# Kernel tuning notes

Hardware: AMD Instinct MI355X
Metric: run time of the kernel (lower is better)

Reference implementation:

```python
import jax, jax.numpy as jnp
import numpy as np

E = 8          # num_ensemble
S = 512        # state_dim
A = 64         # action_dim
H = 2048       # hidden_dim
L = 3          # num_layers - 1 residual hidden blocks
B = 8192
LN_EPS = 1e-5


def _xavier(key, shape, gain=1.0):
    fan_in, fan_out = shape[-2], shape[-1]
    a = gain * np.sqrt(6.0 / (fan_in + fan_out))
    return jax.random.uniform(key, shape, jnp.float32, -a, a)


def setup_inputs() -> dict:
    key = jax.random.key(0)
    ks = jax.random.split(key, 12)
    inp = {
        "state": jax.random.normal(ks[0], (B, S), jnp.float32),
        "action": jax.random.normal(ks[1], (B, A), jnp.float32),
        # input projection
        "W_in": _xavier(ks[2], (E, S + A, H)),
        "b_in": jnp.zeros((E, H), jnp.float32),
        "g_in": jnp.ones((E, H), jnp.float32),
        "be_in": jnp.zeros((E, H), jnp.float32),
        # hidden residual blocks
        "W_h": _xavier(ks[3], (E, L, H, H)),
        "b_h": jnp.zeros((E, L, H), jnp.float32),
        "g_h": jnp.ones((E, L, H), jnp.float32),
        "be_h": jnp.zeros((E, L, H), jnp.float32),
        # output heads
        "W_state": _xavier(ks[4], (E, H, S), gain=0.1),
        "b_state": jnp.zeros((E, S), jnp.float32),
        "W_rew": _xavier(ks[5], (E, H, 1)),
        "b_rew": jnp.zeros((E, 1), jnp.float32),
        "W_done": _xavier(ks[6], (E, H, 1)),
        "b_done": jnp.zeros((E, 1), jnp.float32),
    }
    return inp


def _layernorm(x, g, b):
    # x: [E, B, H]; g, b: [E, 1, H]
    mu = jnp.mean(x, axis=-1, keepdims=True)
    var = jnp.mean(jnp.square(x - mu), axis=-1, keepdims=True)
    return (x - mu) * jax.lax.rsqrt(var + LN_EPS) * g + b


def reference(state, action, W_in, b_in, g_in, be_in, W_h, b_h, g_h, be_h,
              W_state, b_state, W_rew, b_rew, W_done, b_done):
    x = jnp.concatenate([state, action], axis=-1)  # [B, S+A]
    # input proj for all heads: [E, B, H]
    h = jnp.einsum('bi,eih->ebh', x, W_in) + b_in[:, None, :]
    h = jax.nn.gelu(_layernorm(h, g_in[:, None, :], be_in[:, None, :]), approximate=False)
    for l in range(L):
        z = jnp.einsum('ebh,ehk->ebk', h, W_h[:, l]) + b_h[:, l, None, :]
        z = jax.nn.gelu(_layernorm(z, g_h[:, l, None, :], be_h[:, l, None, :]), approximate=False)
        h = z + h
    next_states = state[None] + jnp.einsum('ebh,ehs->ebs', h, W_state) + b_state[:, None, :]
    rewards = jnp.einsum('ebh,eho->ebo', h, W_rew) + b_rew[:, None, :]
    dones = jax.nn.sigmoid(jnp.einsum('ebh,eho->ebo', h, W_done) + b_done[:, None, :])
    mean_state = jnp.mean(next_states, axis=0)          # [B, S]
    mean_reward = jnp.mean(rewards, axis=0)             # [B, 1]
    mean_done = jnp.mean(dones, axis=0)                 # [B, 1]
    # torch.var default is unbiased (correction=1)
    var_state = jnp.var(next_states, axis=0, ddof=1)
    uncertainty = jnp.mean(var_state, axis=-1)          # [B]
    return (mean_state, mean_reward, mean_done, uncertainty)
```

## Files before the change

### kernel.cpp

```cpp
#include <hip/hip_runtime.h>
#include <stdint.h>

#define B_SZ  8192
#define S_DIM 512
#define H_DIM 2048
#define KIN   576
#define OUT_MS 4194304

typedef unsigned short u16;
typedef u16   u16x8 __attribute__((ext_vector_type(8)));
typedef u16   u16x4 __attribute__((ext_vector_type(4)));
typedef short s16x8 __attribute__((ext_vector_type(8)));
typedef float f32x4 __attribute__((ext_vector_type(4)));

__device__ __forceinline__ float b2f(u16 u) {
    union { unsigned int i; float f; } v; v.i = ((unsigned int)u) << 16; return v.f;
}
__device__ __forceinline__ u16 f2b(float f) {
    union { float f; unsigned int i; } v; v.f = f;
    unsigned int u = v.i;
    return (u16)((u + 0x7FFFu + ((u >> 16) & 1u)) >> 16);
}
__device__ __forceinline__ float gelu_f(float y) {
    const float t = __expf(-1.5957691216f * y * (1.0f + 0.044715f * y * y));
    return y / (1.0f + t);
}

__device__ __forceinline__ void gload_lds16(const void* gp, void* lp) {
    __builtin_amdgcn_global_load_lds(
        (const __attribute__((address_space(1))) unsigned int*)gp,
        (__attribute__((address_space(3))) unsigned int*)(unsigned int)(uintptr_t)lp,
        16, 0, 0);
}

#define MFMA __builtin_amdgcn_mfma_f32_16x16x32_bf16

__global__ __launch_bounds__(256) void k_concat(
    const float* __restrict__ state, const float* __restrict__ action,
    u16* __restrict__ xb)
{
    int idx = blockIdx.x * 256 + threadIdx.x;
    int b = idx / KIN, c = idx - b * KIN;
    float v = (c < S_DIM) ? state[(size_t)b * S_DIM + c]
                          : action[(size_t)b * 64 + (c - S_DIM)];
    xb[idx] = f2b(v);
}

__global__ __launch_bounds__(256) void k_cast(
    const float* __restrict__ p0, const float* __restrict__ p1,
    const float* __restrict__ p2, const float* __restrict__ p3,
    const float* __restrict__ p4, const float* __restrict__ p5,
    u16* __restrict__ dst)
{
    int i = blockIdx.x * 256 + threadIdx.x;
    float v;
    if      (i < 16384)  v = p0[i];
    else if (i < 32768)  v = p1[i - 16384];
    else if (i < 81920)  v = p2[i - 32768];
    else if (i < 131072) v = p3[i - 81920];
    else if (i < 147456) v = p4[i - 131072];
    else                 v = p5[i - 147456];
    dst[i] = f2b(v);
}

__global__ __launch_bounds__(256) void k_transpose(
    const float* __restrict__ src, u16* __restrict__ dst, int R, int C)
{
    __shared__ float tile[32][33];
    const int tx = threadIdx.x, ty = threadIdx.y;
    const int c0 = blockIdx.x * 32, r0 = blockIdx.y * 32;
    const size_t mo = (size_t)blockIdx.z * R * C;
    src += mo; dst += mo;
#pragma unroll
    for (int j = 0; j < 4; ++j)
        tile[ty + j * 8][tx] = src[(size_t)(r0 + ty + j * 8) * C + c0 + tx];
    __syncthreads();
#pragma unroll
    for (int j = 0; j < 4; ++j)
        dst[(size_t)(c0 + ty + j * 8) * R + r0 + tx] = f2b(tile[tx][ty + j * 8]);
}

template<int MODE>
__global__ __launch_bounds__(512, 2) void k_gemm256(
    const u16* __restrict__ A, size_t sAe,
    const u16* __restrict__ Bt, size_t sBe,
    const float* __restrict__ bias, int sbE,
    void* __restrict__ Zv, size_t sZe,
    const float* __restrict__ st, float* __restrict__ sum_o, float* __restrict__ sq_o,
    int N, int K)
{
    __shared__ __align__(16) u16 lds[2][32768];
    const int t = threadIdx.x;
    const int lane = t & 63;
    const int wid = t >> 6;
    const int wm = wid >> 2, wn = wid & 3;

    const int gx = gridDim.x, gy = gridDim.y;
    const int linb = blockIdx.x + gx * (blockIdx.y + gy * blockIdx.z);
    const int x  = linb & 7;
    const int s  = linb >> 3;
    const int m_ = (gx * gy) >> 3;
    const int bz = s / m_;
    const int r_ = s - bz * m_;
    const int p_ = r_ / gy;
    const int by = r_ - p_ * gy;
    const int bx = x * (gx >> 3) + p_;
    const int m0 = bx * 256, n0 = by * 256;

    const u16* Ab = A + (size_t)bz * sAe + (size_t)m0 * K;
    const u16* Bb = Bt + (size_t)bz * sBe + (size_t)n0 * K;

    const int srow = t >> 3;
    const int scol = (((t & 7) ^ (srow & 7)) * 8);
    u16* lbase = &lds[0][0];
    const int ldst = srow * 64 + (t & 7) * 8;
    const int NT = K >> 6;
    const int NT2 = NT >> 1;

    const u16* gp_[2][4];
#pragma unroll
    for (int r = 0; r < 4; ++r) {
        gp_[0][r] = Ab + (size_t)srow * K + scol + (size_t)(r * 64) * K;
        gp_[1][r] = Bb + (size_t)srow * K + scol + (size_t)(r * 64) * K;
    }
#define STG(RELT, MAT, R)                                                  \
    gload_lds16(gp_[MAT][R] + (RELT) * 64,                                 \
                lbase + (((RELT) & 1) * 32768 + (MAT) * 16384 + (R) * 4096) + ldst)

    const int fr = lane & 15, hi = lane >> 4;
    const int cswz = (fr & 7) << 4;
    const int ac0 = (hi * 16) ^ cswz;
    const int ac1 = (64 + hi * 16) ^ cswz;
    const int ar0 = (wm * 128 + fr) * 128;
    const int ar1 = (wm * 128 + 16 + fr) * 128;
    int boff[4][2];
#pragma unroll
    for (int nj = 0; nj < 4; ++nj) {
        const int br_ = (wn * 64 + nj * 16 + fr) * 128;
        boff[nj][0] = br_ + ac0;
        boff[nj][1] = br_ + ac1;
    }

    f32x4 acc[8][4];
#pragma unroll
    for (int i = 0; i < 8; ++i)
#pragma unroll
        for (int j = 0; j < 4; ++j) acc[i][j] = (f32x4){0.f, 0.f, 0.f, 0.f};

    s16x8 bfrag[4][2];
    s16x8 af[4];

    const char* LA0 = (const char*)lbase;
    const char* LB0 = LA0 + 32768;
    const char* LA1 = LA0 + 65536;
    const char* LB1 = LA1 + 32768;

#define LOADB(LBx)                                                        \
    _Pragma("unroll") for (int nj = 0; nj < 4; ++nj) {                    \
        bfrag[nj][0] = *(const s16x8*)((LBx) + boff[nj][0]);              \
        bfrag[nj][1] = *(const s16x8*)((LBx) + boff[nj][1]);              \
    }
#define LOADA(LAx, Q)                                                     \
    af[0] = *(const s16x8*)((LAx) + (Q) * 4096 + ar0 + ac0);              \
    af[1] = *(const s16x8*)((LAx) + (Q) * 4096 + ar0 + ac1);              \
    af[2] = *(const s16x8*)((LAx) + (Q) * 4096 + ar1 + ac0);              \
    af[3] = *(const s16x8*)((LAx) + (Q) * 4096 + ar1 + ac1);
#define DOMFMA(Q)                                                         \
    __builtin_amdgcn_s_barrier();                                         \
    asm volatile("s_waitcnt lgkmcnt(0)" ::: "memory");                    \
    __builtin_amdgcn_sched_barrier(0);                                    \
    __builtin_amdgcn_s_setprio(1);                                        \
    _Pragma("unroll") for (int nj = 0; nj < 4; ++nj) {                    \
        acc[2*(Q)][nj]   = MFMA(bfrag[nj][0], af[0], acc[2*(Q)][nj], 0, 0, 0);   \
        acc[2*(Q)][nj]   = MFMA(bfrag[nj][1], af[1], acc[2*(Q)][nj], 0, 0, 0);   \
        acc[2*(Q)+1][nj] = MFMA(bfrag[nj][0], af[2], acc[2*(Q)+1][nj], 0, 0, 0); \
        acc[2*(Q)+1][nj] = MFMA(bfrag[nj][1], af[3], acc[2*(Q)+1][nj], 0, 0, 0); \
    }                                                                     \
    __builtin_amdgcn_s_setprio(0);
#define WAITV(COND)                                                       \
    if (COND) { asm volatile("s_waitcnt vmcnt(6)" ::: "memory"); }        \
    else      { asm volatile("s_waitcnt vmcnt(0)" ::: "memory"); }        \
    __builtin_amdgcn_sched_barrier(0);

    STG(0, 1, 0); STG(0, 1, 1); STG(0, 1, 2); STG(0, 1, 3);
    STG(0, 0, 0); STG(0, 0, 2); STG(0, 0, 1); STG(0, 0, 3);
    STG(1, 1, 0); STG(1, 1, 1); STG(1, 1, 2); STG(1, 1, 3);
    STG(1, 0, 0); STG(1, 0, 2);
    asm volatile("s_waitcnt vmcnt(6)" ::: "memory");
    __builtin_amdgcn_sched_barrier(0);
    __builtin_amdgcn_s_barrier();

    for (int i2 = 0; i2 < NT2; ++i2) {
        const bool h0 = 2 * i2 + 2 < NT, h1 = 2 * i2 + 3 < NT;
        LOADB(LB0) LOADA(LA0, 0)
        STG(1, 0, 1); STG(1, 0, 3);
        DOMFMA(0)
        __builtin_amdgcn_s_barrier();
        LOADA(LA0, 1)
        if (h0) { STG(2, 1, 0); STG(2, 1, 1); }
        DOMFMA(1)
        __builtin_amdgcn_s_barrier();
        LOADA(LA0, 2)
        if (h0) { STG(2, 1, 2); STG(2, 1, 3); }
        DOMFMA(2)
        __builtin_amdgcn_s_barrier();
        LOADA(LA0, 3)
        if (h0) { STG(2, 0, 0); STG(2, 0, 2); }
        DOMFMA(3)
        WAITV(h0)
        __builtin_amdgcn_s_barrier();
        LOADB(LB1) LOADA(LA1, 0)
        if (h0) { STG(2, 0, 1); STG(2, 0, 3); }
        DOMFMA(0)
        __builtin_amdgcn_s_barrier();
        LOADA(LA1, 1)
        if (h1) { STG(3, 1, 0); STG(3, 1, 1); }
        DOMFMA(1)
        __builtin_amdgcn_s_barrier();
        LOADA(LA1, 2)
        if (h1) { STG(3, 1, 2); STG(3, 1, 3); }
        DOMFMA(2)
        __builtin_amdgcn_s_barrier();
        LOADA(LA1, 3)
        if (h1) { STG(3, 0, 0); STG(3, 0, 2); }
        DOMFMA(3)
        WAITV(h1)
        __builtin_amdgcn_s_barrier();
#pragma unroll
        for (int r = 0; r < 4; ++r) { gp_[0][r] += 128; gp_[1][r] += 128; }
    }
    if (NT & 1) {
        LOADB(LB0) LOADA(LA0, 0) DOMFMA(0)
        __builtin_amdgcn_s_barrier();
        LOADA(LA0, 1) DOMFMA(1)
        __builtin_amdgcn_s_barrier();
        LOADA(LA0, 2) DOMFMA(2)
        __builtin_amdgcn_s_barrier();
        LOADA(LA0, 3) DOMFMA(3)
    }
#undef LOADB
#undef LOADA
#undef DOMFMA
#undef WAITV
#undef STG

    const float* biasp = bias + (size_t)bz * sbE;
    f32x4 bias4[4];
#pragma unroll
    for (int nj = 0; nj < 4; ++nj)
        bias4[nj] = *(const f32x4*)&biasp[n0 + wn * 64 + nj * 16 + hi * 4];
#pragma unroll
    for (int mi = 0; mi < 8; ++mi) {
        const int row = m0 + wm * 128 + mi * 16 + fr;
#pragma unroll
        for (int nj = 0; nj < 4; ++nj) {
            const int cb = n0 + wn * 64 + nj * 16 + hi * 4;
            const size_t idx = (size_t)row * N + cb;
            if (MODE == 0) {
                u16x4 o;
#pragma unroll
                for (int r = 0; r < 4; ++r) o[r] = f2b(acc[mi][nj][r] + bias4[nj][r]);
                *(u16x4*)&((u16*)Zv)[(size_t)bz * sZe + idx] = o;
            } else if (MODE == 1) {
                const f32x4 sv = *(const f32x4*)&st[idx];
                f32x4 c;
#pragma unroll
                for (int r = 0; r < 4; ++r) c[r] = sv[r] + acc[mi][nj][r] + bias4[nj][r];
                *(f32x4*)&((float*)Zv)[(size_t)bz * sZe + idx] = c;
            } else {
                const f32x4 sv = *(const f32x4*)&st[idx];
                f32x4 s1 = *(const f32x4*)&sum_o[idx];
                f32x4 s2 = *(const f32x4*)&sq_o[idx];
#pragma unroll
                for (int r = 0; r < 4; ++r) {
                    const float c = sv[r] + acc[mi][nj][r] + bias4[nj][r];
                    s1[r] += c; s2[r] += c * c;
                }
                *(f32x4*)&sum_o[idx] = s1;
                *(f32x4*)&sq_o[idx] = s2;
            }
        }
    }
}

template<int RES, int FIN>
__global__ __launch_bounds__(256) void k_ln(
    const u16* __restrict__ z, u16* __restrict__ h,
    const u16* __restrict__ g, const u16* __restrict__ be, int egb,
    const u16* __restrict__ wr, const u16* __restrict__ wd,
    const float* __restrict__ br, const float* __restrict__ bd,
    float* __restrict__ sum_rew, float* __restrict__ sum_done)
{
    const int lane = threadIdx.x & 63;
    const int w = threadIdx.x >> 6;
    const int e = blockIdx.z;
    const int row0 = blockIdx.x * 8 + w * 2;
    const size_t base0 = ((size_t)e * B_SZ + row0) * H_DIM;
    const u16* gp = g + (size_t)e * egb;
    const u16* bp = be + (size_t)e * egb;

    u16x8 zv[2][4], gv[4], bv[4], hv[2][4];
#pragma unroll
    for (int j = 0; j < 4; ++j) {
        const int c = j * 512 + lane * 8;
        zv[0][j] = *(const u16x8*)&z[base0 + c];
        zv[1][j] = *(const u16x8*)&z[base0 + H_DIM + c];
        gv[j] = *(const u16x8*)&gp[c];
        bv[j] = *(const u16x8*)&bp[c];
        if (RES) {
            hv[0][j] = *(const u16x8*)&h[base0 + c];
            hv[1][j] = *(const u16x8*)&h[base0 + H_DIM + c];
        }
    }
    float s0 = 0.f, q0 = 0.f, s1 = 0.f, q1 = 0.f;
#pragma unroll
    for (int j = 0; j < 4; ++j)
#pragma unroll
        for (int k = 0; k < 8; ++k) {
            const float f0 = b2f(zv[0][j][k]); s0 += f0; q0 += f0 * f0;
            const float f1 = b2f(zv[1][j][k]); s1 += f1; q1 += f1 * f1;
        }
#pragma unroll
    for (int o = 32; o; o >>= 1) {
        s0 += __shfl_xor(s0, o); q0 += __shfl_xor(q0, o);
        s1 += __shfl_xor(s1, o); q1 += __shfl_xor(q1, o);
    }
    const float mu0 = s0 * (1.0f / H_DIM);
    const float rs0 = rsqrtf(q0 * (1.0f / H_DIM) - mu0 * mu0 + 1e-5f);
    const float mu1 = s1 * (1.0f / H_DIM);
    const float rs1 = rsqrtf(q1 * (1.0f / H_DIM) - mu1 * mu1 + 1e-5f);

    float dr0 = 0.f, dd0 = 0.f, dr1 = 0.f, dd1 = 0.f;
#pragma unroll
    for (int j = 0; j < 4; ++j) {
        const int c = j * 512 + lane * 8;
        u16x8 wrv, wdv;
        if (FIN) {
            wrv = *(const u16x8*)&wr[(size_t)e * H_DIM + c];
            wdv = *(const u16x8*)&wd[(size_t)e * H_DIM + c];
        }
        u16x8 ov0, ov1;
#pragma unroll
        for (int k = 0; k < 8; ++k) {
            const float gk = b2f(gv[j][k]), bk = b2f(bv[j][k]);
            const float y0 = (b2f(zv[0][j][k]) - mu0) * rs0 * gk + bk;
            const float y1 = (b2f(zv[1][j][k]) - mu1) * rs1 * gk + bk;
            float g0 = gelu_f(y0), g1 = gelu_f(y1);
            if (RES) { g0 += b2f(hv[0][j][k]); g1 += b2f(hv[1][j][k]); }
            if (FIN) {
                const float wrk = b2f(wrv[k]), wdk = b2f(wdv[k]);
                dr0 += g0 * wrk; dd0 += g0 * wdk;
                dr1 += g1 * wrk; dd1 += g1 * wdk;
            }
            ov0[k] = f2b(g0); ov1[k] = f2b(g1);
        }
        *(u16x8*)&h[base0 + c] = ov0;
        *(u16x8*)&h[base0 + H_DIM + c] = ov1;
    }
    if (FIN) {
#pragma unroll
        for (int o = 32; o; o >>= 1) {
            dr0 += __shfl_xor(dr0, o); dd0 += __shfl_xor(dd0, o);
            dr1 += __shfl_xor(dr1, o); dd1 += __shfl_xor(dd1, o);
        }
        if (lane == 0) {
            atomicAdd(&sum_rew[row0], dr0 + br[e]);
            atomicAdd(&sum_done[row0], 1.0f / (1.0f + __expf(-(dd0 + bd[e]))));
            atomicAdd(&sum_rew[row0 + 1], dr1 + br[e]);
            atomicAdd(&sum_done[row0 + 1], 1.0f / (1.0f + __expf(-(dd1 + bd[e]))));
        }
    }
}

__global__ __launch_bounds__(256) void k_rewdone(
    const u16* __restrict__ hB, const float* __restrict__ Wr, const float* __restrict__ Wd,
    const float* __restrict__ br, const float* __restrict__ bd,
    float* __restrict__ sum_rew, float* __restrict__ sum_done)
{
    const int e = blockIdx.z;
    const int lane = threadIdx.x & 63;
    const int b = blockIdx.x * 4 + (threadIdx.x >> 6);
    const u16* hrow = hB + ((size_t)e * B_SZ + b) * H_DIM;
    const float* wr_ = Wr + (size_t)e * H_DIM;
    const float* wd_ = Wd + (size_t)e * H_DIM;
    float dr = 0.f, dd = 0.f;
#pragma unroll
    for (int j = 0; j < 4; ++j) {
        const int o = j * 512 + lane * 8;
        u16x8 hv = *(const u16x8*)&hrow[o];
#pragma unroll
        for (int k = 0; k < 8; ++k) {
            const float f = b2f(hv[k]);
            dr += f * wr_[o + k];
            dd += f * wd_[o + k];
        }
    }
#pragma unroll
    for (int o = 32; o; o >>= 1) { dr += __shfl_xor(dr, o); dd += __shfl_xor(dd, o); }
    if (lane == 0) {
        atomicAdd(&sum_rew[b], dr + br[e]);
        atomicAdd(&sum_done[b], 1.0f / (1.0f + expf(-(dd + bd[e]))));
    }
}

template<int FB>
__global__ __launch_bounds__(256) void k_final(
    const float* __restrict__ P, const float* __restrict__ sum_st,
    const float* __restrict__ sq_st, const float* __restrict__ sum_rew,
    const float* __restrict__ sum_done, float* __restrict__ out)
{
    const int b = blockIdx.x, t = threadIdx.x;
    float vs = 0.f;
#pragma unroll
    for (int k = 0; k < 2; ++k) {
        const int s = t + k * 256;
        const size_t i = (size_t)b * S_DIM + s;
        float S1, S2;
        if (FB == 0) {
            S1 = 0.f; S2 = 0.f;
#pragma unroll
            for (int e = 0; e < 8; ++e) {
                const float c = P[(size_t)e * OUT_MS + i];
                S1 += c; S2 += c * c;
            }
        } else { S1 = sum_st[i]; S2 = sq_st[i]; }
        out[i] = S1 * 0.125f;
        vs += (S2 - S1 * S1 * 0.125f) * (1.0f / 7.0f);
    }
#pragma unroll
    for (int o = 32; o; o >>= 1) vs += __shfl_xor(vs, o);
    __shared__ float rv[4];
    if ((t & 63) == 0) rv[t >> 6] = vs;
    __syncthreads();
    if (t == 0) {
        const float tot = rv[0] + rv[1] + rv[2] + rv[3];
        out[OUT_MS + b] = sum_rew[b] * 0.125f;
        out[OUT_MS + B_SZ + b] = sum_done[b] * 0.125f;
        out[OUT_MS + 2 * B_SZ + b] = tot * (1.0f / S_DIM);
    }
}

extern "C" void kernel_launch(void* const* d_in, const int* in_sizes, int n_in,
                              void* d_out, int out_size, void* d_ws, size_t ws_size,
                              hipStream_t stream) {
    (void)in_sizes; (void)n_in; (void)out_size;
    const float* state   = (const float*)d_in[0];
    const float* action  = (const float*)d_in[1];
    const float* W_in    = (const float*)d_in[2];
    const float* b_in    = (const float*)d_in[3];
    const float* g_in    = (const float*)d_in[4];
    const float* be_in   = (const float*)d_in[5];
    const float* W_h     = (const float*)d_in[6];
    const float* b_h     = (const float*)d_in[7];
    const float* g_h     = (const float*)d_in[8];
    const float* be_h    = (const float*)d_in[9];
    const float* W_state = (const float*)d_in[10];
    const float* b_state = (const float*)d_in[11];
    const float* W_rew   = (const float*)d_in[12];
    const float* b_rew   = (const float*)d_in[13];
    const float* W_done  = (const float*)d_in[14];
    const float* b_done  = (const float*)d_in[15];
    float* out = (float*)d_out;

    char* ws = (char*)d_ws;
    size_t off = 0;
    auto alloc = [&](size_t bytes) -> void* {
        void* p = ws + off; off += (bytes + 255) & ~((size_t)255); return p;
    };
    const size_t BH = (size_t)B_SZ * H_DIM;
    u16*   xb      = (u16*)alloc((size_t)B_SZ * KIN * 2);
    u16*   Wt_in   = (u16*)alloc((size_t)8 * H_DIM * KIN * 2);
    u16*   Wt_h    = (u16*)alloc((size_t)24 * H_DIM * H_DIM * 2);
    u16*   Wt_st   = (u16*)alloc((size_t)8 * S_DIM * H_DIM * 2);
    u16*   gb16    = (u16*)alloc((size_t)163840 * 2);
    float* sum_st  = (float*)alloc((size_t)B_SZ * S_DIM * 4);
    float* sq_st   = (float*)alloc((size_t)B_SZ * S_DIM * 4);
    float* sum_rew = (float*)alloc((size_t)B_SZ * 4);
    float* sum_done= (float*)alloc((size_t)B_SZ * 4);
    const size_t fixed = off;
    const int EB = (ws_size >= fixed + 2ULL * 8 * BH * 2) ? 8 : 1;
    u16*   hbuf    = (u16*)alloc((size_t)EB * BH * 2);
    u16*   zbuf    = (u16*)alloc((size_t)EB * BH * 2);
    float* Pbuf    = (float*)zbuf;

    u16* g16_in = gb16;
    u16* be16_in = gb16 + 16384;
    u16* g16_h = gb16 + 32768;
    u16* be16_h = gb16 + 81920;
    u16* wr16 = gb16 + 131072;
    u16* wd16 = gb16 + 147456;

    if (EB == 8) {
        hipMemsetAsync(sum_rew, 0, 2 * (size_t)B_SZ * 4, stream);
    } else {
        hipMemsetAsync(sum_st, 0, (2 * (size_t)B_SZ * S_DIM + 2 * B_SZ) * 4, stream);
    }

    k_concat<<<dim3((B_SZ * KIN) / 256), dim3(256), 0, stream>>>(state, action, xb);
    k_cast<<<dim3(640), dim3(256), 0, stream>>>(g_in, be_in, g_h, be_h, W_rew, W_done, gb16);
    k_transpose<<<dim3(H_DIM / 32, KIN / 32, 8),    dim3(32, 8), 0, stream>>>(W_in, Wt_in, KIN, H_DIM);
    k_transpose<<<dim3(H_DIM / 32, H_DIM / 32, 24), dim3(32, 8), 0, stream>>>(W_h, Wt_h, H_DIM, H_DIM);
    k_transpose<<<dim3(S_DIM / 32, H_DIM / 32, 8),  dim3(32, 8), 0, stream>>>(W_state, Wt_st, H_DIM, S_DIM);

    for (int e0 = 0; e0 < 8; e0 += EB) {
        const dim3 gH(32, 8, EB), gS(32, 2, EB), gL(B_SZ / 8, 1, EB), gF(B_SZ / 4, 1, EB);
        k_gemm256<0><<<gH, 512, 0, stream>>>(
            xb, 0, Wt_in + (size_t)e0 * H_DIM * KIN, (size_t)H_DIM * KIN,
            b_in + (size_t)e0 * H_DIM, H_DIM, zbuf, BH,
            nullptr, nullptr, nullptr, H_DIM, KIN);
        k_ln<0, 0><<<gL, 256, 0, stream>>>(zbuf, hbuf,
            g16_in + (size_t)e0 * H_DIM, be16_in + (size_t)e0 * H_DIM, H_DIM,
            nullptr, nullptr, nullptr, nullptr, nullptr, nullptr);
        for (int l = 0; l < 3; ++l) {
            k_gemm256<0><<<gH, 512, 0, stream>>>(
                hbuf, BH, Wt_h + ((size_t)e0 * 3 + l) * H_DIM * H_DIM, (size_t)3 * H_DIM * H_DIM,
                b_h + (size_t)(e0 * 3 + l) * H_DIM, 3 * H_DIM, zbuf, BH,
                nullptr, nullptr, nullptr, H_DIM, H_DIM);
            if (EB == 8 && l == 2) {
                k_ln<1, 1><<<gL, 256, 0, stream>>>(zbuf, hbuf,
                    g16_h + (size_t)(e0 * 3 + l) * H_DIM, be16_h + (size_t)(e0 * 3 + l) * H_DIM,
                    3 * H_DIM, wr16, wd16, b_rew, b_done, sum_rew, sum_done);
            } else {
                k_ln<1, 0><<<gL, 256, 0, stream>>>(zbuf, hbuf,
                    g16_h + (size_t)(e0 * 3 + l) * H_DIM, be16_h + (size_t)(e0 * 3 + l) * H_DIM,
                    3 * H_DIM, nullptr, nullptr, nullptr, nullptr, nullptr, nullptr);
            }
        }
        if (EB == 8) {
            k_gemm256<1><<<gS, 512, 0, stream>>>(
                hbuf, BH, Wt_st, (size_t)S_DIM * H_DIM,
                b_state, S_DIM, (void*)Pbuf, (size_t)OUT_MS,
                state, nullptr, nullptr, S_DIM, H_DIM);
        } else {
            k_gemm256<2><<<gS, 512, 0, stream>>>(
                hbuf, BH, Wt_st + (size_t)e0 * S_DIM * H_DIM, (size_t)S_DIM * H_DIM,
                b_state + (size_t)e0 * S_DIM, S_DIM, (void*)zbuf, 0,
                state, sum_st, sq_st, S_DIM, H_DIM);
            k_rewdone<<<gF, 256, 0, stream>>>(hbuf,
                W_rew + (size_t)e0 * H_DIM, W_done + (size_t)e0 * H_DIM,
                b_rew + e0, b_done + e0, sum_rew, sum_done);
        }
    }
    if (EB == 8)
        k_final<0><<<dim3(B_SZ), dim3(256), 0, stream>>>(Pbuf, nullptr, nullptr, sum_rew, sum_done, out);
    else
        k_final<1><<<dim3(B_SZ), dim3(256), 0, stream>>>(nullptr, sum_st, sq_st, sum_rew, sum_done, out);
}
```

Baseline: 2.610 ms.

## Pre-swizzle weights into MFMA fragment layout and switch to 32x32x16 MFMA

Replaces the weight transpose with a kernel that packs each weight matrix directly into per-lane 32x32x16 MFMA fragment order. The GEMM then reads B fragments straight from global memory into registers, double-buffered, and stages only A through LDS using a three-slab ring. The inner loop moves from 16x16x32 to 32x32x16 bf16 MFMA, and the epilogue is rewritten for the new accumulator layout. This is meant to cut LDS traffic and barrier work for B and raise MFMA efficiency. In exchange, B loads hit global and L2 directly, register pressure rises, and the previous hand-tuned schedule is dropped.

```diff
diff --git a/kernel.cpp b/kernel.cpp
--- a/kernel.cpp
+++ b/kernel.cpp
@@ -12,6 +12,7 @@
 typedef u16   u16x4 __attribute__((ext_vector_type(4)));
 typedef short s16x8 __attribute__((ext_vector_type(8)));
 typedef float f32x4 __attribute__((ext_vector_type(4)));
+typedef float f32x16 __attribute__((ext_vector_type(16)));
 
 __device__ __forceinline__ float b2f(u16 u) {
     union { unsigned int i; float f; } v; v.i = ((unsigned int)u) << 16; return v.f;
@@ -33,7 +34,7 @@
         16, 0, 0);
 }
 
-#define MFMA __builtin_amdgcn_mfma_f32_16x16x32_bf16
+#define MFMA32 __builtin_amdgcn_mfma_f32_32x32x16_bf16
 
 __global__ __launch_bounds__(256) void k_concat(
     const float* __restrict__ state, const float* __restrict__ action,
@@ -63,33 +64,33 @@
     dst[i] = f2b(v);
 }
 
-__global__ __launch_bounds__(256) void k_transpose(
-    const float* __restrict__ src, u16* __restrict__ dst, int R, int C)
-{
-    __shared__ float tile[32][33];
-    const int tx = threadIdx.x, ty = threadIdx.y;
-    const int c0 = blockIdx.x * 32, r0 = blockIdx.y * 32;
-    const size_t mo = (size_t)blockIdx.z * R * C;
-    src += mo; dst += mo;
-#pragma unroll
-    for (int j = 0; j < 4; ++j)
-        tile[ty + j * 8][tx] = src[(size_t)(r0 + ty + j * 8) * C + c0 + tx];
-    __syncthreads();
-#pragma unroll
-    for (int j = 0; j < 4; ++j)
-        dst[(size_t)(c0 + ty + j * 8) * R + r0 + tx] = f2b(tile[tx][ty + j * 8]);
+__global__ __launch_bounds__(256) void k_wfrag(
+    const float* __restrict__ W, u16* __restrict__ Wf, int Kd, int Nd)
+{
+    const int KS = Kd >> 4;
+    const size_t mo = (size_t)blockIdx.z * Kd * Nd;
+    const int gid = blockIdx.x * 256 + threadIdx.x;
+    const int lane = gid & 63, fid = gid >> 6;
+    const int ks = fid % KS, nc = fid / KS;
+    const int n = nc * 32 + (lane & 31);
+    const int k0 = ks * 16 + (lane >> 5) * 8;
+    const float* src = W + mo + (size_t)k0 * Nd + n;
+    u16x8 o;
+#pragma unroll
+    for (int j = 0; j < 8; ++j) o[j] = f2b(src[(size_t)j * Nd]);
+    *(u16x8*)&Wf[mo + (size_t)fid * 512 + lane * 8] = o;
 }
 
 template<int MODE>
 __global__ __launch_bounds__(512, 2) void k_gemm256(
     const u16* __restrict__ A, size_t sAe,
-    const u16* __restrict__ Bt, size_t sBe,
+    const u16* __restrict__ Wf, size_t sBe,
     const float* __restrict__ bias, int sbE,
     void* __restrict__ Zv, size_t sZe,
     const float* __restrict__ st, float* __restrict__ sum_o, float* __restrict__ sq_o,
     int N, int K)
 {
-    __shared__ __align__(16) u16 lds[2][32768];
+    __shared__ __align__(16) u16 lds[3][16384];
     const int t = threadIdx.x;
     const int lane = t & 63;
     const int wid = t >> 6;
@@ -108,176 +109,129 @@
     const int m0 = bx * 256, n0 = by * 256;
 
     const u16* Ab = A + (size_t)bz * sAe + (size_t)m0 * K;
-    const u16* Bb = Bt + (size_t)bz * sBe + (size_t)n0 * K;
-
     const int srow = t >> 3;
-    const int scol = (((t & 7) ^ (srow & 7)) * 8);
-    u16* lbase = &lds[0][0];
+    const int scol = ((t & 7) ^ (srow & 7)) * 8;
     const int ldst = srow * 64 + (t & 7) * 8;
-    const int NT = K >> 6;
-    const int NT2 = NT >> 1;
-
-    const u16* gp_[2][4];
-#pragma unroll
-    for (int r = 0; r < 4; ++r) {
-        gp_[0][r] = Ab + (size_t)srow * K + scol + (size_t)(r * 64) * K;
-        gp_[1][r] = Bb + (size_t)srow * K + scol + (size_t)(r * 64) * K;
-    }
-#define STG(RELT, MAT, R)                                                  \
-    gload_lds16(gp_[MAT][R] + (RELT) * 64,                                 \
-                lbase + (((RELT) & 1) * 32768 + (MAT) * 16384 + (R) * 4096) + ldst)
-
-    const int fr = lane & 15, hi = lane >> 4;
-    const int cswz = (fr & 7) << 4;
-    const int ac0 = (hi * 16) ^ cswz;
-    const int ac1 = (64 + hi * 16) ^ cswz;
-    const int ar0 = (wm * 128 + fr) * 128;
-    const int ar1 = (wm * 128 + 16 + fr) * 128;
-    int boff[4][2];
-#pragma unroll
-    for (int nj = 0; nj < 4; ++nj) {
-        const int br_ = (wn * 64 + nj * 16 + fr) * 128;
-        boff[nj][0] = br_ + ac0;
-        boff[nj][1] = br_ + ac1;
-    }
-
-    f32x4 acc[8][4];
-#pragma unroll
-    for (int i = 0; i < 8; ++i)
-#pragma unroll
-        for (int j = 0; j < 4; ++j) acc[i][j] = (f32x4){0.f, 0.f, 0.f, 0.f};
-
-    s16x8 bfrag[4][2];
-    s16x8 af[4];
-
-    const char* LA0 = (const char*)lbase;
-    const char* LB0 = LA0 + 32768;
-    const char* LA1 = LA0 + 65536;
-    const char* LB1 = LA1 + 32768;
-
-#define LOADB(LBx)                                                        \
-    _Pragma("unroll") for (int nj = 0; nj < 4; ++nj) {                    \
-        bfrag[nj][0] = *(const s16x8*)((LBx) + boff[nj][0]);              \
-        bfrag[nj][1] = *(const s16x8*)((LBx) + boff[nj][1]);              \
-    }
-#define LOADA(LAx, Q)                                                     \
-    af[0] = *(const s16x8*)((LAx) + (Q) * 4096 + ar0 + ac0);              \
-    af[1] = *(const s16x8*)((LAx) + (Q) * 4096 + ar0 + ac1);              \
-    af[2] = *(const s16x8*)((LAx) + (Q) * 4096 + ar1 + ac0);              \
-    af[3] = *(const s16x8*)((LAx) + (Q) * 4096 + ar1 + ac1);
-#define DOMFMA(Q)                                                         \
-    __builtin_amdgcn_s_barrier();                                         \
-    asm volatile("s_waitcnt lgkmcnt(0)" ::: "memory");                    \
-    __builtin_amdgcn_sched_barrier(0);                                    \
-    __builtin_amdgcn_s_setprio(1);                                        \
-    _Pragma("unroll") for (int nj = 0; nj < 4; ++nj) {                    \
-        acc[2*(Q)][nj]   = MFMA(bfrag[nj][0], af[0], acc[2*(Q)][nj], 0, 0, 0);   \
-        acc[2*(Q)][nj]   = MFMA(bfrag[nj][1], af[1], acc[2*(Q)][nj], 0, 0, 0);   \
-        acc[2*(Q)+1][nj] = MFMA(bfrag[nj][0], af[2], acc[2*(Q)+1][nj], 0, 0, 0); \
-        acc[2*(Q)+1][nj] = MFMA(bfrag[nj][1], af[3], acc[2*(Q)+1][nj], 0, 0, 0); \
-    }                                                                     \
-    __builtin_amdgcn_s_setprio(0);
-#define WAITV(COND)                                                       \
-    if (COND) { asm volatile("s_waitcnt vmcnt(6)" ::: "memory"); }        \
-    else      { asm volatile("s_waitcnt vmcnt(0)" ::: "memory"); }        \
-    __builtin_amdgcn_sched_barrier(0);
-
-    STG(0, 1, 0); STG(0, 1, 1); STG(0, 1, 2); STG(0, 1, 3);
-    STG(0, 0, 0); STG(0, 0, 2); STG(0, 0, 1); STG(0, 0, 3);
-    STG(1, 1, 0); STG(1, 1, 1); STG(1, 1, 2); STG(1, 1, 3);
-    STG(1, 0, 0); STG(1, 0, 2);
-    asm volatile("s_waitcnt vmcnt(6)" ::: "memory");
-    __builtin_amdgcn_sched_barrier(0);
-    __builtin_amdgcn_s_barrier();
-
-    for (int i2 = 0; i2 < NT2; ++i2) {
-        const bool h0 = 2 * i2 + 2 < NT, h1 = 2 * i2 + 3 < NT;
-        LOADB(LB0) LOADA(LA0, 0)
-        STG(1, 0, 1); STG(1, 0, 3);
-        DOMFMA(0)
-        __builtin_amdgcn_s_barrier();
-        LOADA(LA0, 1)
-        if (h0) { STG(2, 1, 0); STG(2, 1, 1); }
-        DOMFMA(1)
-        __builtin_amdgcn_s_barrier();
-        LOADA(LA0, 2)
-        if (h0) { STG(2, 1, 2); STG(2, 1, 3); }
-        DOMFMA(2)
-        __builtin_amdgcn_s_barrier();
-        LOADA(LA0, 3)
-        if (h0) { STG(2, 0, 0); STG(2, 0, 2); }
-        DOMFMA(3)
-        WAITV(h0)
-        __builtin_amdgcn_s_barrier();
-        LOADB(LB1) LOADA(LA1, 0)
-        if (h0) { STG(2, 0, 1); STG(2, 0, 3); }
-        DOMFMA(0)
-        __builtin_amdgcn_s_barrier();
-        LOADA(LA1, 1)
-        if (h1) { STG(3, 1, 0); STG(3, 1, 1); }
-        DOMFMA(1)
-        __builtin_amdgcn_s_barrier();
-        LOADA(LA1, 2)
-        if (h1) { STG(3, 1, 2); STG(3, 1, 3); }
-        DOMFMA(2)
-        __builtin_amdgcn_s_barrier();
-        LOADA(LA1, 3)
-        if (h1) { STG(3, 0, 0); STG(3, 0, 2); }
-        DOMFMA(3)
-        WAITV(h1)
-        __builtin_amdgcn_s_barrier();
-#pragma unroll
-        for (int r = 0; r < 4; ++r) { gp_[0][r] += 128; gp_[1][r] += 128; }
-    }
-    if (NT & 1) {
-        LOADB(LB0) LOADA(LA0, 0) DOMFMA(0)
-        __builtin_amdgcn_s_barrier();
-        LOADA(LA0, 1) DOMFMA(1)
-        __builtin_amdgcn_s_barrier();
-        LOADA(LA0, 2) DOMFMA(2)
-        __builtin_amdgcn_s_barrier();
-        LOADA(LA0, 3) DOMFMA(3)
-    }
-#undef LOADB
-#undef LOADA
-#undef DOMFMA
-#undef WAITV
-#undef STG
+    const int NT = K >> 6, KS = K >> 4;
+
+    auto STGA = [&](int kt, u16* slab) {
+#pragma unroll
+        for (int r = 0; r < 4; ++r)
+            gload_lds16(Ab + (size_t)(r * 64 + srow) * K + kt * 64 + scol,
+                        slab + r * 4096 + ldst);
+    };
+
+    const u16* wfb = Wf + (size_t)bz * sBe
+                   + ((size_t)((n0 >> 5) + wn * 2) * KS) * 512 + (size_t)lane * 8;
+#define LOADBF(bf, ksb)                                                      \
+    _Pragma("unroll") for (int ni = 0; ni < 2; ++ni)                         \
+    _Pragma("unroll") for (int ss = 0; ss < 4; ++ss)                         \
+        bf[ni][ss] = *(const s16x8*)(wfb + ((size_t)ni * KS + (ksb) + ss) * 512);
+
+    const int l31 = lane & 31, lh = lane >> 5, s7 = l31 & 7;
+    int baseA[4], ko[4];
+#pragma unroll
+    for (int mi = 0; mi < 4; ++mi)
+        baseA[mi] = (wm * 2 + (mi >> 1)) * 8192 + ((mi & 1) * 32 + l31) * 128;
+#pragma unroll
+    for (int q = 0; q < 4; ++q) ko[q] = ((2 * q + lh) ^ s7) << 4;
+
+    f32x16 acc[4][2];
+#pragma unroll
+    for (int mi = 0; mi < 4; ++mi)
+#pragma unroll
+        for (int ni = 0; ni < 2; ++ni)
+#pragma unroll
+            for (int e = 0; e < 16; ++e) acc[mi][ni][e] = 0.f;
+
+    s16x8 bf0[2][4], bf1[2][4];
+    u16* laA = (u16*)&lds[0][0];
+    u16* laB = (u16*)&lds[1][0];
+    u16* laC = (u16*)&lds[2][0];
+
+    STGA(0, laA);
+    STGA(1, laB);
+    LOADBF(bf0, 0)
+
+#define TILE(KT, BFC, BFN, LAc, LAn2) {                                      \
+    const bool h1 = (KT) + 1 < NT, h2 = (KT) + 2 < NT;                       \
+    __builtin_amdgcn_s_barrier();                                            \
+    if (h2) STGA((KT) + 2, LAn2);                                            \
+    if (h1) { LOADBF(BFN, ((KT) + 1) * 4) }                                  \
+    if (h2)      { asm volatile("s_waitcnt vmcnt(12)" ::: "memory"); }       \
+    else if (h1) { asm volatile("s_waitcnt vmcnt(8)"  ::: "memory"); }       \
+    else         { asm volatile("s_waitcnt vmcnt(0)"  ::: "memory"); }       \
+    __builtin_amdgcn_sched_barrier(0);                                       \
+    const char* LAp = (const char*)(LAc);                                    \
+    _Pragma("unroll") for (int q = 0; q < 4; ++q) {                          \
+        s16x8 a0 = *(const s16x8*)(LAp + baseA[0] + ko[q]);                  \
+        s16x8 a1 = *(const s16x8*)(LAp + baseA[1] + ko[q]);                  \
+        s16x8 a2 = *(const s16x8*)(LAp + baseA[2] + ko[q]);                  \
+        s16x8 a3 = *(const s16x8*)(LAp + baseA[3] + ko[q]);                  \
+        __builtin_amdgcn_s_setprio(1);                                       \
+        acc[0][0] = MFMA32(BFC[0][q], a0, acc[0][0], 0, 0, 0);               \
+        acc[0][1] = MFMA32(BFC[1][q], a0, acc[0][1], 0, 0, 0);               \
+        acc[1][0] = MFMA32(BFC[0][q], a1, acc[1][0], 0, 0, 0);               \
+        acc[1][1] = MFMA32(BFC[1][q], a1, acc[1][1], 0, 0, 0);               \
+        acc[2][0] = MFMA32(BFC[0][q], a2, acc[2][0], 0, 0, 0);               \
+        acc[2][1] = MFMA32(BFC[1][q], a2, acc[2][1], 0, 0, 0);               \
+        acc[3][0] = MFMA32(BFC[0][q], a3, acc[3][0], 0, 0, 0);               \
+        acc[3][1] = MFMA32(BFC[1][q], a3, acc[3][1], 0, 0, 0);               \
+        __builtin_amdgcn_s_setprio(0);                                       \
+    } }
+
+    int kt = 0;
+    for (; kt + 1 < NT; kt += 2) {
+        TILE(kt, bf0, bf1, laA, laC)
+        u16* tp = laA; laA = laB; laB = laC; laC = tp;
+        TILE(kt + 1, bf1, bf0, laA, laC)
+        tp = laA; laA = laB; laB = laC; laC = tp;
+    }
+    if (kt < NT) { TILE(kt, bf0, bf1, laA, laC) }
+#undef TILE
+#undef LOADBF
 
     const float* biasp = bias + (size_t)bz * sbE;
-    f32x4 bias4[4];
-#pragma unroll
-    for (int nj = 0; nj < 4; ++nj)
-        bias4[nj] = *(const f32x4*)&biasp[n0 + wn * 64 + nj * 16 + hi * 4];
-#pragma unroll
-    for (int mi = 0; mi < 8; ++mi) {
-        const int row = m0 + wm * 128 + mi * 16 + fr;
-#pragma unroll
-        for (int nj = 0; nj < 4; ++nj) {
-            const int cb = n0 + wn * 64 + nj * 16 + hi * 4;
-            const size_t idx = (size_t)row * N + cb;
-            if (MODE == 0) {
-                u16x4 o;
-#pragma unroll
-                for (int r = 0; r < 4; ++r) o[r] = f2b(acc[mi][nj][r] + bias4[nj][r]);
-                *(u16x4*)&((u16*)Zv)[(size_t)bz * sZe + idx] = o;
-            } else if (MODE == 1) {
-                const f32x4 sv = *(const f32x4*)&st[idx];
-                f32x4 c;
-#pragma unroll
-                for (int r = 0; r < 4; ++r) c[r] = sv[r] + acc[mi][nj][r] + bias4[nj][r];
-                *(f32x4*)&((float*)Zv)[(size_t)bz * sZe + idx] = c;
-            } else {
-                const f32x4 sv = *(const f32x4*)&st[idx];
-                f32x4 s1 = *(const f32x4*)&sum_o[idx];
-                f32x4 s2 = *(const f32x4*)&sq_o[idx];
-#pragma unroll
-                for (int r = 0; r < 4; ++r) {
-                    const float c = sv[r] + acc[mi][nj][r] + bias4[nj][r];
-                    s1[r] += c; s2[r] += c * c;
+    f32x4 bias4[2][4];
+#pragma unroll
+    for (int ni = 0; ni < 2; ++ni)
+#pragma unroll
+        for (int rq = 0; rq < 4; ++rq)
+            bias4[ni][rq] = *(const f32x4*)&biasp[n0 + wn * 64 + ni * 32 + rq * 8 + lh * 4];
+#pragma unroll
+    for (int mi = 0; mi < 4; ++mi) {
+        const int row = m0 + wm * 128 + mi * 32 + l31;
+#pragma unroll
+        for (int ni = 0; ni < 2; ++ni) {
+#pragma unroll
+            for (int rq = 0; rq < 4; ++rq) {
+                const int cb = n0 + wn * 64 + ni * 32 + rq * 8 + lh * 4;
+                const size_t idx = (size_t)row * N + cb;
+                if (MODE == 0) {
+                    u16x4 o;
+#pragma unroll
+                    for (int j = 0; j < 4; ++j)
+                        o[j] = f2b(acc[mi][ni][rq * 4 + j] + bias4[ni][rq][j]);
+                    *(u16x4*)&((u16*)Zv)[(size_t)bz * sZe + idx] = o;
+                } else if (MODE == 1) {
+                    const f32x4 sv = *(const f32x4*)&st[idx];
+                    f32x4 c;
+#pragma unroll
+                    for (int j = 0; j < 4; ++j)
+                        c[j] = sv[j] + acc[mi][ni][rq * 4 + j] + bias4[ni][rq][j];
+                    *(f32x4*)&((float*)Zv)[(size_t)bz * sZe + idx] = c;
+                } else {
+                    const f32x4 sv = *(const f32x4*)&st[idx];
+                    f32x4 s1 = *(const f32x4*)&sum_o[idx];
+                    f32x4 s2 = *(const f32x4*)&sq_o[idx];
+#pragma unroll
+                    for (int j = 0; j < 4; ++j) {
+                        const float c = sv[j] + acc[mi][ni][rq * 4 + j] + bias4[ni][rq][j];
+                        s1[j] += c; s2[j] += c * c;
+                    }
+                    *(f32x4*)&sum_o[idx] = s1;
+                    *(f32x4*)&sq_o[idx] = s2;
                 }
-                *(f32x4*)&sum_o[idx] = s1;
-                *(f32x4*)&sq_o[idx] = s2;
             }
         }
     }
@@ -469,9 +423,9 @@
     };
     const size_t BH = (size_t)B_SZ * H_DIM;
     u16*   xb      = (u16*)alloc((size_t)B_SZ * KIN * 2);
-    u16*   Wt_in   = (u16*)alloc((size_t)8 * H_DIM * KIN * 2);
-    u16*   Wt_h    = (u16*)alloc((size_t)24 * H_DIM * H_DIM * 2);
-    u16*   Wt_st   = (u16*)alloc((size_t)8 * S_DIM * H_DIM * 2);
+    u16*   Wf_in   = (u16*)alloc((size_t)8 * H_DIM * KIN * 2);
+    u16*   Wf_h    = (u16*)alloc((size_t)24 * H_DIM * H_DIM * 2);
+    u16*   Wf_st   = (u16*)alloc((size_t)8 * S_DIM * H_DIM * 2);
     u16*   gb16    = (u16*)alloc((size_t)163840 * 2);
     float* sum_st  = (float*)alloc((size_t)B_SZ * S_DIM * 4);
     float* sq_st   = (float*)alloc((size_t)B_SZ * S_DIM * 4);
@@ -498,14 +452,14 @@
 
     k_concat<<<dim3((B_SZ * KIN) / 256), dim3(256), 0, stream>>>(state, action, xb);
     k_cast<<<dim3(640), dim3(256), 0, stream>>>(g_in, be_in, g_h, be_h, W_rew, W_done, gb16);
-    k_transpose<<<dim3(H_DIM / 32, KIN / 32, 8),    dim3(32, 8), 0, stream>>>(W_in, Wt_in, KIN, H_DIM);
-    k_transpose<<<dim3(H_DIM / 32, H_DIM / 32, 24), dim3(32, 8), 0, stream>>>(W_h, Wt_h, H_DIM, H_DIM);
-    k_transpose<<<dim3(S_DIM / 32, H_DIM / 32, 8),  dim3(32, 8), 0, stream>>>(W_state, Wt_st, H_DIM, S_DIM);
+    k_wfrag<<<dim3(576, 1, 8),   dim3(256), 0, stream>>>(W_in, Wf_in, KIN, H_DIM);
+    k_wfrag<<<dim3(2048, 1, 24), dim3(256), 0, stream>>>(W_h, Wf_h, H_DIM, H_DIM);
+    k_wfrag<<<dim3(512, 1, 8),   dim3(256), 0, stream>>>(W_state, Wf_st, H_DIM, S_DIM);
 
     for (int e0 = 0; e0 < 8; e0 += EB) {
         const dim3 gH(32, 8, EB), gS(32, 2, EB), gL(B_SZ / 8, 1, EB), gF(B_SZ / 4, 1, EB);
         k_gemm256<0><<<gH, 512, 0, stream>>>(
-            xb, 0, Wt_in + (size_t)e0 * H_DIM * KIN, (size_t)H_DIM * KIN,
+            xb, 0, Wf_in + (size_t)e0 * H_DIM * KIN, (size_t)H_DIM * KIN,
             b_in + (size_t)e0 * H_DIM, H_DIM, zbuf, BH,
             nullptr, nullptr, nullptr, H_DIM, KIN);
         k_ln<0, 0><<<gL, 256, 0, stream>>>(zbuf, hbuf,
@@ -513,7 +467,7 @@
             nullptr, nullptr, nullptr, nullptr, nullptr, nullptr);
         for (int l = 0; l < 3; ++l) {
             k_gemm256<0><<<gH, 512, 0, stream>>>(
-                hbuf, BH, Wt_h + ((size_t)e0 * 3 + l) * H_DIM * H_DIM, (size_t)3 * H_DIM * H_DIM,
+                hbuf, BH, Wf_h + ((size_t)e0 * 3 + l) * H_DIM * H_DIM, (size_t)3 * H_DIM * H_DIM,
                 b_h + (size_t)(e0 * 3 + l) * H_DIM, 3 * H_DIM, zbuf, BH,
                 nullptr, nullptr, nullptr, H_DIM, H_DIM);
             if (EB == 8 && l == 2) {
@@ -528,12 +482,12 @@
         }
         if (EB == 8) {
             k_gemm256<1><<<gS, 512, 0, stream>>>(
-                hbuf, BH, Wt_st, (size_t)S_DIM * H_DIM,
+                hbuf, BH, Wf_st, (size_t)S_DIM * H_DIM,
                 b_state, S_DIM, (void*)Pbuf, (size_t)OUT_MS,
                 state, nullptr, nullptr, S_DIM, H_DIM);
         } else {
             k_gemm256<2><<<gS, 512, 0, stream>>>(
-                hbuf, BH, Wt_st + (size_t)e0 * S_DIM * H_DIM, (size_t)S_DIM * H_DIM,
+                hbuf, BH, Wf_st + (size_t)e0 * S_DIM * H_DIM, (size_t)S_DIM * H_DIM,
                 b_state + (size_t)e0 * S_DIM, S_DIM, (void*)zbuf, 0,
                 state, sum_st, sq_st, S_DIM, H_DIM);
             k_rewdone<<<gF, 256, 0, stream>>>(hbuf,
```

Measured after the change: 3.142 ms. 1.2x slower.

## Triple-buffer A tiles and double-buffer B tiles in GEMM LDS pipeline

Applied to the files above, without the earlier changes.

The GEMM main loop changes from a 2x-unrolled double-buffered schedule to a single-step loop. A tiles are held in three LDS slabs and prefetched two K-tiles ahead, while B tiles are double-buffered and prefetched one tile ahead. Slab pointers rotate each iteration. The aim is to give global-to-LDS loads of A more time to land before they are needed. In exchange, LDS use grows to 160KB, the full per-CU budget, and the rotating pointers make LDS addresses runtime values, which may add address arithmetic and register pressure.

```diff
diff --git a/kernel.cpp b/kernel.cpp
--- a/kernel.cpp
+++ b/kernel.cpp
@@ -89,7 +89,7 @@
     const float* __restrict__ st, float* __restrict__ sum_o, float* __restrict__ sq_o,
     int N, int K)
 {
-    __shared__ __align__(16) u16 lds[2][32768];
+    __shared__ __align__(16) u16 lds[5][16384];
     const int t = threadIdx.x;
     const int lane = t & 63;
     const int wid = t >> 6;
@@ -112,20 +112,15 @@
 
     const int srow = t >> 3;
     const int scol = (((t & 7) ^ (srow & 7)) * 8);
-    u16* lbase = &lds[0][0];
     const int ldst = srow * 64 + (t & 7) * 8;
     const int NT = K >> 6;
-    const int NT2 = NT >> 1;
-
-    const u16* gp_[2][4];
-#pragma unroll
-    for (int r = 0; r < 4; ++r) {
-        gp_[0][r] = Ab + (size_t)srow * K + scol + (size_t)(r * 64) * K;
-        gp_[1][r] = Bb + (size_t)srow * K + scol + (size_t)(r * 64) * K;
-    }
-#define STG(RELT, MAT, R)                                                  \
-    gload_lds16(gp_[MAT][R] + (RELT) * 64,                                 \
-                lbase + (((RELT) & 1) * 32768 + (MAT) * 16384 + (R) * 4096) + ldst)
+
+    const u16* gA = Ab + (size_t)srow * K + scol;
+    const u16* gB = Bb + (size_t)srow * K + scol;
+    auto STG = [&](int kt, int mat, int r, u16* slab) {
+        const u16* gp = (mat ? gB : gA) + (size_t)(r * 64) * K + kt * 64;
+        gload_lds16(gp, slab + r * 4096 + ldst);
+    };
 
     const int fr = lane & 15, hi = lane >> 4;
     const int cswz = (fr & 7) << 4;
@@ -150,21 +145,22 @@
     s16x8 bfrag[4][2];
     s16x8 af[4];
 
-    const char* LA0 = (const char*)lbase;
-    const char* LB0 = LA0 + 32768;
-    const char* LA1 = LA0 + 65536;
-    const char* LB1 = LA1 + 32768;
-
-#define LOADB(LBx)                                                        \
+    u16* pa0 = &lds[0][0];
+    u16* pa1 = &lds[1][0];
+    u16* pa2 = &lds[2][0];
+    u16* pb0 = &lds[3][0];
+    u16* pb1 = &lds[4][0];
+
+#define LOADB(PB)                                                         \
     _Pragma("unroll") for (int nj = 0; nj < 4; ++nj) {                    \
-        bfrag[nj][0] = *(const s16x8*)((LBx) + boff[nj][0]);              \
-        bfrag[nj][1] = *(const s16x8*)((LBx) + boff[nj][1]);              \
-    }
-#define LOADA(LAx, Q)                                                     \
-    af[0] = *(const s16x8*)((LAx) + (Q) * 4096 + ar0 + ac0);              \
-    af[1] = *(const s16x8*)((LAx) + (Q) * 4096 + ar0 + ac1);              \
-    af[2] = *(const s16x8*)((LAx) + (Q) * 4096 + ar1 + ac0);              \
-    af[3] = *(const s16x8*)((LAx) + (Q) * 4096 + ar1 + ac1);
+        bfrag[nj][0] = *(const s16x8*)((const char*)(PB) + boff[nj][0]);  \
+        bfrag[nj][1] = *(const s16x8*)((const char*)(PB) + boff[nj][1]);  \
+    }
+#define LOADA(PA, Q)                                                      \
+    af[0] = *(const s16x8*)((const char*)(PA) + (Q) * 4096 + ar0 + ac0);  \
+    af[1] = *(const s16x8*)((const char*)(PA) + (Q) * 4096 + ar0 + ac1);  \
+    af[2] = *(const s16x8*)((const char*)(PA) + (Q) * 4096 + ar1 + ac0);  \
+    af[3] = *(const s16x8*)((const char*)(PA) + (Q) * 4096 + ar1 + ac1);
 #define DOMFMA(Q)                                                         \
     __builtin_amdgcn_s_barrier();                                         \
     asm volatile("s_waitcnt lgkmcnt(0)" ::: "memory");                    \
@@ -177,72 +173,45 @@
         acc[2*(Q)+1][nj] = MFMA(bfrag[nj][1], af[3], acc[2*(Q)+1][nj], 0, 0, 0); \
     }                                                                     \
     __builtin_amdgcn_s_setprio(0);
-#define WAITV(COND)                                                       \
-    if (COND) { asm volatile("s_waitcnt vmcnt(6)" ::: "memory"); }        \
-    else      { asm volatile("s_waitcnt vmcnt(0)" ::: "memory"); }        \
-    __builtin_amdgcn_sched_barrier(0);
-
-    STG(0, 1, 0); STG(0, 1, 1); STG(0, 1, 2); STG(0, 1, 3);
-    STG(0, 0, 0); STG(0, 0, 2); STG(0, 0, 1); STG(0, 0, 3);
-    STG(1, 1, 0); STG(1, 1, 1); STG(1, 1, 2); STG(1, 1, 3);
-    STG(1, 0, 0); STG(1, 0, 2);
-    asm volatile("s_waitcnt vmcnt(6)" ::: "memory");
+
+    STG(0, 0, 0, pa0); STG(0, 0, 1, pa0); STG(0, 0, 2, pa0); STG(0, 0, 3, pa0);
+    STG(0, 1, 0, pb0); STG(0, 1, 1, pb0); STG(0, 1, 2, pb0); STG(0, 1, 3, pb0);
+    if (NT > 1) {
+        STG(1, 0, 0, pa1); STG(1, 0, 1, pa1); STG(1, 0, 2, pa1); STG(1, 0, 3, pa1);
+        asm volatile("s_waitcnt vmcnt(4)" ::: "memory");
+    } else {
+        asm volatile("s_waitcnt vmcnt(0)" ::: "memory");
+    }
     __builtin_amdgcn_sched_barrier(0);
     __builtin_amdgcn_s_barrier();
 
-    for (int i2 = 0; i2 < NT2; ++i2) {
-        const bool h0 = 2 * i2 + 2 < NT, h1 = 2 * i2 + 3 < NT;
-        LOADB(LB0) LOADA(LA0, 0)
-        STG(1, 0, 1); STG(1, 0, 3);
+    for (int kt = 0; kt < NT; ++kt) {
+        const bool h1 = kt + 1 < NT, h2 = kt + 2 < NT;
+        LOADB(pb0) LOADA(pa0, 0)
+        if (h1) { STG(kt + 1, 1, 0, pb1); STG(kt + 1, 1, 1, pb1);
+                  STG(kt + 1, 1, 2, pb1); STG(kt + 1, 1, 3, pb1); }
         DOMFMA(0)
         __builtin_amdgcn_s_barrier();
-        LOADA(LA0, 1)
-        if (h0) { STG(2, 1, 0); STG(2, 1, 1); }
+        LOADA(pa0, 1)
+        if (h2) { STG(kt + 2, 0, 0, pa2); STG(kt + 2, 0, 2, pa2); }
         DOMFMA(1)
         __builtin_amdgcn_s_barrier();
-        LOADA(LA0, 2)
-        if (h0) { STG(2, 1, 2); STG(2, 1, 3); }
+        LOADA(pa0, 2)
+        if (h2) { STG(kt + 2, 0, 1, pa2); STG(kt + 2, 0, 3, pa2); }
         DOMFMA(2)
         __builtin_amdgcn_s_barrier();
-        LOADA(LA0, 3)
-        if (h0) { STG(2, 0, 0); STG(2, 0, 2); }
+        LOADA(pa0, 3)
         DOMFMA(3)
-        WAITV(h0)
+        if (h2) { asm volatile("s_waitcnt vmcnt(4)" ::: "memory"); }
+        else    { asm volatile("s_waitcnt vmcnt(0)" ::: "memory"); }
+        __builtin_amdgcn_sched_barrier(0);
         __builtin_amdgcn_s_barrier();
-        LOADB(LB1) LOADA(LA1, 0)
-        if (h0) { STG(2, 0, 1); STG(2, 0, 3); }
-        DOMFMA(0)
-        __builtin_amdgcn_s_barrier();
-        LOADA(LA1, 1)
-        if (h1) { STG(3, 1, 0); STG(3, 1, 1); }
-        DOMFMA(1)
-        __builtin_amdgcn_s_barrier();
-        LOADA(LA1, 2)
-        if (h1) { STG(3, 1, 2); STG(3, 1, 3); }
-        DOMFMA(2)
-        __builtin_amdgcn_s_barrier();
-        LOADA(LA1, 3)
-        if (h1) { STG(3, 0, 0); STG(3, 0, 2); }
-        DOMFMA(3)
-        WAITV(h1)
-        __builtin_amdgcn_s_barrier();
-#pragma unroll
-        for (int r = 0; r < 4; ++r) { gp_[0][r] += 128; gp_[1][r] += 128; }
-    }
-    if (NT & 1) {
-        LOADB(LB0) LOADA(LA0, 0) DOMFMA(0)
-        __builtin_amdgcn_s_barrier();
-        LOADA(LA0, 1) DOMFMA(1)
-        __builtin_amdgcn_s_barrier();
-        LOADA(LA0, 2) DOMFMA(2)
-        __builtin_amdgcn_s_barrier();
-        LOADA(LA0, 3) DOMFMA(3)
+        u16* ta = pa0; pa0 = pa1; pa1 = pa2; pa2 = ta;
+        u16* tb = pb0; pb0 = pb1; pb1 = tb;
     }
 #undef LOADB
 #undef LOADA
 #undef DOMFMA
-#undef WAITV
-#undef STG
 
     const float* biasp = bias + (size_t)bz * sbE;
     f32x4 bias4[4];
```

Result: no change. 2.655 ms (+1.7%).
